# Kernel tuning notes

Hardware: AMD Instinct MI355X
Metric: run time of the kernel (lower is better)

## Reference

```python
import jax, jax.numpy as jnp
import numpy as np

B, S, D = 16, 2048, 256

def setup_inputs() -> dict:
    key = jax.random.key(0)
    ks = jax.random.split(key, 7)
    scale = 1.0 / np.sqrt(D)
    return {
        "x": jax.random.normal(ks[0], (B, S, D), dtype=jnp.float32),
        "Wq": jax.random.normal(ks[1], (D, D), dtype=jnp.float32) * scale,
        "bq": jax.random.normal(ks[2], (D,), dtype=jnp.float32) * 0.01,
        "Wk": jax.random.normal(ks[3], (D, D), dtype=jnp.float32) * scale,
        "bk": jax.random.normal(ks[4], (D,), dtype=jnp.float32) * 0.01,
        "Wv": jax.random.normal(ks[5], (D, D), dtype=jnp.float32) * scale,
        "bv": jax.random.normal(ks[6], (D,), dtype=jnp.float32) * 0.01,
    }

def reference(x, Wq, bq, Wk, bk, Wv, bv):
    # q,k,v: [B,S,D]
    q = x @ Wq + bq
    k = x @ Wk + bk
    v = x @ Wv + bv
    inv_sqrt_d = jnp.asarray(1.0 / np.sqrt(x.shape[-1]), dtype=x.dtype)
    energy = jnp.einsum('bqd,bkd->bqk', q, k) * inv_sqrt_d  # [B,S,S]
    attn = jax.nn.softmax(energy, axis=-1)
    weighted = jnp.einsum('bqk,bkd->bqd', attn, v)  # [B,S,D]
    return weighted.sum(axis=1)  # [B,D]
```

## Files before the change

kernel.cpp:

```cpp
#include <hip/hip_runtime.h>
#include <hip/hip_bf16.h>

typedef __bf16 bf16_t;
typedef bf16_t bf16x8 __attribute__((ext_vector_type(8)));
typedef bf16_t bf16x4 __attribute__((ext_vector_type(4)));
typedef float  f32x4  __attribute__((ext_vector_type(4)));

constexpr int S = 2048, D = 256;


__device__ __forceinline__ float fast_exp2(float x) {
    return __builtin_amdgcn_exp2f(x);
}

__global__ void wt_kernel(const float* __restrict__ Wq, const float* __restrict__ Wk,
                          bf16_t* __restrict__ wtf) {
    int idx = blockIdx.x * 256 + threadIdx.x;
    int w    = idx >> 13;
    int rem  = idx & 8191;
    int nt   = rem >> 9;
    int rem2 = rem & 511;
    int ks   = rem2 >> 6;
    int lane = rem2 & 63;
    int lm = lane & 15, lg = lane >> 4;
    const float* Wsrc = (w == 0) ? Wq : Wk;
    int col = nt * 16 + lm, krow = ks * 32 + lg * 8;
    bf16x8 o;
#pragma unroll
    for (int j = 0; j < 8; j++) o[j] = (bf16_t)Wsrc[(krow + j) * 256 + col];
    *(bf16x8*)(wtf + (size_t)idx * 8) = o;
}

__global__ __launch_bounds__(256) void xconv_kernel(
    const float* __restrict__ x, bf16_t* __restrict__ xf) {
    __shared__ bf16_t xt[4][4096];
    int tid = threadIdx.x, wave = tid >> 6, lane = tid & 63;
    int qb = blockIdx.x * 4 + wave;
    const float* xr = x + (size_t)qb * 16 * 256;
    bf16_t* buf = xt[wave];
    int ks = lane >> 3, lg = (lane & 7) >> 1, j = (lane & 1) * 4;
#pragma unroll
    for (int rr = 0; rr < 16; rr++) {
        float4 f = *(const float4*)(xr + rr * 256 + lane * 4);
        bf16x4 o;
        o[0] = (bf16_t)f.x; o[1] = (bf16_t)f.y; o[2] = (bf16_t)f.z; o[3] = (bf16_t)f.w;
        *(bf16x4*)&buf[(ks * 64 + lg * 16 + rr) * 8 + j] = o;
    }
    bf16_t* dst = xf + (size_t)qb * 4096;
#pragma unroll
    for (int k2 = 0; k2 < 8; k2++) {
        bf16x8 v = *(const bf16x8*)&buf[k2 * 512 + lane * 8];
        *(bf16x8*)(dst + k2 * 512 + lane * 8) = v;
    }
}

__global__ __launch_bounds__(256, 2) void proj_kernel(
    const bf16_t* __restrict__ xf, const bf16_t* __restrict__ wtf,
    const float* __restrict__ bq, const float* __restrict__ bk,
    bf16_t* __restrict__ qo, bf16_t* __restrict__ ko) {
    __shared__ bf16_t bst[32768];
    __shared__ bf16_t sb_all[4][1152];
    int w    = blockIdx.y;
    int tid  = threadIdx.x;
    int wave = tid >> 6, lane = tid & 63, lm = lane & 15, lg = lane >> 4;
    int rowb = blockIdx.x >> 1;
    int colh = blockIdx.x & 1;
    int rowg = wave >> 1, colg = wave & 1;
    const float* bias = (w == 0) ? bq : bk;

    {
        const bf16_t* src = wtf + w * 65536 + (size_t)colh * 32768;
#pragma unroll
        for (int rnd = 0; rnd < 4; rnd++) {
            bf16x8 tmp[4];
#pragma unroll
            for (int u = 0; u < 4; u++)
                tmp[u] = *(const bf16x8*)(src + (size_t)((rnd * 4 + u) * 256 + tid) * 8);
#pragma unroll
            for (int u = 0; u < 4; u++)
                *(bf16x8*)&bst[(size_t)((rnd * 4 + u) * 256 + tid) * 8] = tmp[u];
        }
    }

    int qb0 = rowb * 8 + rowg * 4;
    bf16x8 af[4][8];
#pragma unroll
    for (int s = 0; s < 4; s++) {
        const bf16_t* ab = xf + (size_t)(qb0 + s) * 4096;
#pragma unroll
        for (int ks = 0; ks < 8; ks++)
            af[s][ks] = *(const bf16x8*)(ab + ks * 512 + lane * 8);
    }
    __syncthreads();

    f32x4 acc[4][4];
#pragma unroll
    for (int s = 0; s < 4; s++)
#pragma unroll
        for (int nt = 0; nt < 4; nt++) acc[s][nt] = f32x4{0.f, 0.f, 0.f, 0.f};
#pragma unroll
    for (int ks = 0; ks < 8; ks++) {
#pragma unroll
        for (int nt = 0; nt < 4; nt++) {
            bf16x8 bfr = *(const bf16x8*)&bst[(size_t)(((colg * 4 + nt) * 8 + ks) * 512) + lane * 8];
#pragma unroll
            for (int s = 0; s < 4; s++)
                acc[s][nt] = __builtin_amdgcn_mfma_f32_16x16x32_bf16(af[s][ks], bfr, acc[s][nt], 0, 0, 0);
        }
    }

    bf16_t* sb = sb_all[wave];
    bf16_t* dst = (w == 0) ? qo : ko;
    int c0 = colh * 128 + colg * 64;
#pragma unroll
    for (int s = 0; s < 4; s++) {
#pragma unroll
        for (int nt = 0; nt < 4; nt++) {
            int colloc = nt * 16 + lm;
            float bval = bias[c0 + colloc];
#pragma unroll
            for (int r = 0; r < 4; r++)
                sb[(lg * 4 + r) * 72 + colloc] = (bf16_t)(acc[s][nt][r] + bval);
        }
#pragma unroll
        for (int kk = 0; kk < 2; kk++) {
            bf16x8 v8 = *(const bf16x8*)&sb[lm * 72 + kk * 32 + lg * 8];
            *(bf16x8*)(dst + ((size_t)((qb0 + s) * 8 + (c0 >> 5) + kk)) * 512 + lane * 8) = v8;
        }
    }
}

template <int PASS>
__global__ __launch_bounds__(256) void attn_pass(
    const bf16_t* __restrict__ q, const bf16_t* __restrict__ kmat,
    float* __restrict__ lpart, float* __restrict__ wpart) {
    __shared__ bf16_t kst[2][16384];
    __shared__ float  wacc[4][512];

    int tid  = threadIdx.x;
    int wave = tid >> 6, lane = tid & 63, lm = lane & 15, lg = lane >> 4;
    int i    = blockIdx.x;
    int b    = (i & 7) * 2 + ((i >> 8) & 1);
    int qt   = (i >> 3) & 7;
    int kh   = (i >> 6) & 3;

    bf16x8 af[4][8];
#pragma unroll
    for (int s = 0; s < 4; s++) {
        const bf16_t* qb = q + ((size_t)((b * 128 + qt * 16 + wave * 4 + s) * 8)) * 512;
#pragma unroll
        for (int ks = 0; ks < 8; ks++)
            af[s][ks] = *(const bf16x8*)(qb + ks * 512 + lane * 8);
    }

    constexpr float SCL = 0.0625f * 1.44269504f;

    float lr[4][4];
    if (PASS == 2) {
#pragma unroll
        for (int s = 0; s < 4; s++)
#pragma unroll
            for (int r = 0; r < 4; r++) {
                int row = qt * 256 + wave * 64 + s * 16 + lg * 4 + r;
                float l = 0.f;
#pragma unroll
                for (int k2 = 0; k2 < 4; k2++)
                    l += lpart[(size_t)(k2 * 16 + b) * 2048 + row];
                lr[s][r] = -__builtin_log2f(l);
            }
    }

    float lsum[4][4];
#pragma unroll
    for (int s = 0; s < 4; s++)
#pragma unroll
        for (int r = 0; r < 4; r++) lsum[s][r] = 0.f;

    const bf16_t* kb_base = kmat + (size_t)(b * 128 + kh * 32) * 4096;

    bf16x8 stg[8];
#pragma unroll
    for (int u = 0; u < 8; u++)
        stg[u] = *(const bf16x8*)(kb_base + (size_t)(u * 256 + tid) * 8);

    for (int t = 0; t < 8; t++) {
        int p = t & 1;
#pragma unroll
        for (int u = 0; u < 8; u++)
            *(bf16x8*)&kst[p][(u * 256 + tid) * 8] = stg[u];
        if (t < 7) {
#pragma unroll
            for (int u = 0; u < 8; u++)
                stg[u] = *(const bf16x8*)(kb_base + (size_t)(t + 1) * 16384 + (u * 256 + tid) * 8);
        }
        __syncthreads();

#pragma unroll
        for (int h = 0; h < 2; h++) {
            f32x4 sacc[4][2];
#pragma unroll
            for (int s = 0; s < 4; s++) {
                sacc[s][0] = f32x4{0.f, 0.f, 0.f, 0.f};
                sacc[s][1] = f32x4{0.f, 0.f, 0.f, 0.f};
            }
#pragma unroll
            for (int ks = 0; ks < 8; ks++) {
                bf16x8 b0 = *(const bf16x8*)&kst[p][((h * 2 + 0) * 8 + ks) * 512 + lane * 8];
                bf16x8 b1 = *(const bf16x8*)&kst[p][((h * 2 + 1) * 8 + ks) * 512 + lane * 8];
#pragma unroll
                for (int s = 0; s < 4; s++) {
                    sacc[s][0] = __builtin_amdgcn_mfma_f32_16x16x32_bf16(af[s][ks], b0, sacc[s][0], 0, 0, 0);
                    sacc[s][1] = __builtin_amdgcn_mfma_f32_16x16x32_bf16(af[s][ks], b1, sacc[s][1], 0, 0, 0);
                }
            }
            if (PASS == 1) {
#pragma unroll
                for (int s = 0; s < 4; s++)
#pragma unroll
                    for (int j = 0; j < 2; j++)
#pragma unroll
                        for (int r = 0; r < 4; r++)
                            lsum[s][r] += fast_exp2(sacc[s][j][r] * SCL);
            } else {
#pragma unroll
                for (int j = 0; j < 2; j++) {
                    float wv = 0.f;
#pragma unroll
                    for (int s = 0; s < 4; s++)
#pragma unroll
                        for (int r = 0; r < 4; r++)
                            wv += fast_exp2(__builtin_fmaf(sacc[s][j][r], SCL, lr[s][r]));
                    wv += __shfl_xor(wv, 16);
                    wv += __shfl_xor(wv, 32);
                    if (lg == 0) wacc[wave][t * 64 + (h * 2 + j) * 16 + lm] = wv;
                }
            }
        }
        __syncthreads();
    }

    if (PASS == 1) {
#pragma unroll
        for (int s = 0; s < 4; s++)
#pragma unroll
            for (int r = 0; r < 4; r++) {
                float v2 = lsum[s][r];
                v2 += __shfl_xor(v2, 1);
                v2 += __shfl_xor(v2, 2);
                v2 += __shfl_xor(v2, 4);
                v2 += __shfl_xor(v2, 8);
                if (lm == 0) {
                    int row = qt * 256 + wave * 64 + s * 16 + lg * 4 + r;
                    lpart[(size_t)(kh * 16 + b) * 2048 + row] = v2;
                }
            }
    } else {
#pragma unroll
        for (int u = 0; u < 2; u++) {
            int key = u * 256 + tid;
            float sum = wacc[0][key] + wacc[1][key] + wacc[2][key] + wacc[3][key];
            wpart[(size_t)(qt * 16 + b) * 2048 + kh * 512 + key] = sum;
        }
    }
}

__global__ __launch_bounds__(256) void xsum_kernel(
    const float* __restrict__ wpart, const float* __restrict__ x,
    float* __restrict__ gpart) {
    __shared__ float ldsw[128];
    int b = blockIdx.x >> 4, kseg = blockIdx.x & 15, tid = threadIdx.x;
    if (tid < 128) {
        int key = kseg * 128 + tid;
        float s = 0.f;
#pragma unroll
        for (int qt = 0; qt < 8; qt++) s += wpart[(size_t)(qt * 16 + b) * 2048 + key];
        ldsw[tid] = s;
    }
    __syncthreads();
    const float* xb = x + ((size_t)b * 2048 + kseg * 128) * 256;
    float acc = 0.f;
#pragma unroll 8
    for (int t = 0; t < 128; t++) acc += ldsw[t] * xb[(size_t)t * 256 + tid];
    gpart[(size_t)(kseg * 16 + b) * 256 + tid] = acc;
}

__global__ __launch_bounds__(256) void final_kernel(
    const float* __restrict__ gpart, const float* __restrict__ Wv,
    const float* __restrict__ bv, float* __restrict__ out) {
    __shared__ float yl[256];
    int b = blockIdx.x, tid = threadIdx.x;
    float s = 0.f;
#pragma unroll
    for (int ks = 0; ks < 16; ks++) s += gpart[(size_t)(ks * 16 + b) * 256 + tid];
    yl[tid] = s;
    __syncthreads();
    float acc = 0.f;
#pragma unroll 4
    for (int c = 0; c < 256; c++) acc += yl[c] * Wv[c * 256 + tid];
    out[b * 256 + tid] = acc + 2048.0f * bv[tid];
}

extern "C" void kernel_launch(void* const* d_in, const int* in_sizes, int n_in,
                              void* d_out, int out_size, void* d_ws, size_t ws_size,
                              hipStream_t stream) {
    const float* x  = (const float*)d_in[0];
    const float* Wq = (const float*)d_in[1];
    const float* bq = (const float*)d_in[2];
    const float* Wk = (const float*)d_in[3];
    const float* bk = (const float*)d_in[4];
    const float* Wv = (const float*)d_in[5];
    const float* bv = (const float*)d_in[6];
    float* out = (float*)d_out;

    char* ws = (char*)d_ws;
    bf16_t* wtf   = (bf16_t*)(ws);
    bf16_t* xf    = (bf16_t*)(ws + 262144);
    bf16_t* q     = (bf16_t*)(ws + 17039360);
    bf16_t* kmat  = (bf16_t*)(ws + 33816576);
    float*  lpart = (float*) (ws + 50593792);
    float*  wpart = (float*) (ws + 51118080);
    float*  gpart = (float*) (ws + 52166656);

    wt_kernel<<<dim3(64), dim3(256), 0, stream>>>(Wq, Wk, wtf);
    xconv_kernel<<<dim3(512), dim3(256), 0, stream>>>(x, xf);
    proj_kernel<<<dim3(512, 2), dim3(256), 0, stream>>>(xf, wtf, bq, bk, q, kmat);
    attn_pass<1><<<dim3(512), dim3(256), 0, stream>>>(q, kmat, lpart, wpart);
    attn_pass<2><<<dim3(512), dim3(256), 0, stream>>>(q, kmat, lpart, wpart);
    xsum_kernel<<<dim3(256), dim3(256), 0, stream>>>(wpart, x, gpart);
    final_kernel<<<dim3(16), dim3(256), 0, stream>>>(gpart, Wv, bv, out);
}
```

Before: 204.1 us.

## Split attention key range into 16 chunks per block, load K tile once

The attention passes now split the key dimension into 16 chunks of 128 keys instead of 4 chunks of 512, launching 2048 blocks instead of 512. Each block loads its whole 128-key K tile into shared memory once, replacing the double-buffered streaming loop and its per-tile barriers. The aim is better occupancy and more parallelism across the GPU's CUs. In exchange, each block reloads the Q fragments for fewer keys, and pass 2 reads 16 partial row sums per row instead of 4. The lpart buffer grows, so the workspace offsets move.

```diff
diff --git a/kernel.cpp b/kernel.cpp
--- a/kernel.cpp
+++ b/kernel.cpp
@@ -134,15 +134,26 @@
 __global__ __launch_bounds__(256) void attn_pass(
     const bf16_t* __restrict__ q, const bf16_t* __restrict__ kmat,
     float* __restrict__ lpart, float* __restrict__ wpart) {
-    __shared__ bf16_t kst[2][16384];
-    __shared__ float  wacc[4][512];
+    __shared__ bf16_t kst[32768];
+    __shared__ float  wacc[4][128];
 
     int tid  = threadIdx.x;
     int wave = tid >> 6, lane = tid & 63, lm = lane & 15, lg = lane >> 4;
     int i    = blockIdx.x;
-    int b    = (i & 7) * 2 + ((i >> 8) & 1);
+    int b    = (i & 7) * 2 + ((i >> 10) & 1);
     int qt   = (i >> 3) & 7;
-    int kh   = (i >> 6) & 3;
+    int kh   = (i >> 6) & 15;
+
+    {
+        const bf16_t* src = kmat + (size_t)(b * 128 + kh * 8) * 4096;
+        bf16x8 stg[16];
+#pragma unroll
+        for (int u = 0; u < 16; u++)
+            stg[u] = *(const bf16x8*)(src + (size_t)(u * 256 + tid) * 8);
+#pragma unroll
+        for (int u = 0; u < 16; u++)
+            *(bf16x8*)&kst[(u * 256 + tid) * 8] = stg[u];
+    }
 
     bf16x8 af[4][8];
 #pragma unroll
@@ -164,7 +175,7 @@
                 int row = qt * 256 + wave * 64 + s * 16 + lg * 4 + r;
                 float l = 0.f;
 #pragma unroll
-                for (int k2 = 0; k2 < 4; k2++)
+                for (int k2 = 0; k2 < 16; k2++)
                     l += lpart[(size_t)(k2 * 16 + b) * 2048 + row];
                 lr[s][r] = -__builtin_log2f(l);
             }
@@ -176,67 +187,48 @@
 #pragma unroll
         for (int r = 0; r < 4; r++) lsum[s][r] = 0.f;
 
-    const bf16_t* kb_base = kmat + (size_t)(b * 128 + kh * 32) * 4096;
-
-    bf16x8 stg[8];
-#pragma unroll
-    for (int u = 0; u < 8; u++)
-        stg[u] = *(const bf16x8*)(kb_base + (size_t)(u * 256 + tid) * 8);
-
-    for (int t = 0; t < 8; t++) {
-        int p = t & 1;
-#pragma unroll
-        for (int u = 0; u < 8; u++)
-            *(bf16x8*)&kst[p][(u * 256 + tid) * 8] = stg[u];
-        if (t < 7) {
-#pragma unroll
-            for (int u = 0; u < 8; u++)
-                stg[u] = *(const bf16x8*)(kb_base + (size_t)(t + 1) * 16384 + (u * 256 + tid) * 8);
-        }
-        __syncthreads();
-
-#pragma unroll
-        for (int h = 0; h < 2; h++) {
-            f32x4 sacc[4][2];
+    __syncthreads();
+
+#pragma unroll
+    for (int kp = 0; kp < 4; kp++) {
+        f32x4 sacc[4][2];
+#pragma unroll
+        for (int s = 0; s < 4; s++) {
+            sacc[s][0] = f32x4{0.f, 0.f, 0.f, 0.f};
+            sacc[s][1] = f32x4{0.f, 0.f, 0.f, 0.f};
+        }
+#pragma unroll
+        for (int ks = 0; ks < 8; ks++) {
+            bf16x8 b0 = *(const bf16x8*)&kst[((kp * 2 + 0) * 8 + ks) * 512 + lane * 8];
+            bf16x8 b1 = *(const bf16x8*)&kst[((kp * 2 + 1) * 8 + ks) * 512 + lane * 8];
 #pragma unroll
             for (int s = 0; s < 4; s++) {
-                sacc[s][0] = f32x4{0.f, 0.f, 0.f, 0.f};
-                sacc[s][1] = f32x4{0.f, 0.f, 0.f, 0.f};
+                sacc[s][0] = __builtin_amdgcn_mfma_f32_16x16x32_bf16(af[s][ks], b0, sacc[s][0], 0, 0, 0);
+                sacc[s][1] = __builtin_amdgcn_mfma_f32_16x16x32_bf16(af[s][ks], b1, sacc[s][1], 0, 0, 0);
             }
-#pragma unroll
-            for (int ks = 0; ks < 8; ks++) {
-                bf16x8 b0 = *(const bf16x8*)&kst[p][((h * 2 + 0) * 8 + ks) * 512 + lane * 8];
-                bf16x8 b1 = *(const bf16x8*)&kst[p][((h * 2 + 1) * 8 + ks) * 512 + lane * 8];
-#pragma unroll
-                for (int s = 0; s < 4; s++) {
-                    sacc[s][0] = __builtin_amdgcn_mfma_f32_16x16x32_bf16(af[s][ks], b0, sacc[s][0], 0, 0, 0);
-                    sacc[s][1] = __builtin_amdgcn_mfma_f32_16x16x32_bf16(af[s][ks], b1, sacc[s][1], 0, 0, 0);
-                }
+        }
+        if (PASS == 1) {
+#pragma unroll
+            for (int s = 0; s < 4; s++)
+#pragma unroll
+                for (int j = 0; j < 2; j++)
+#pragma unroll
+                    for (int r = 0; r < 4; r++)
+                        lsum[s][r] += fast_exp2(sacc[s][j][r] * SCL);
+        } else {
+#pragma unroll
+            for (int j = 0; j < 2; j++) {
+                float wv = 0.f;
+#pragma unroll
+                for (int s = 0; s < 4; s++)
+#pragma unroll
+                    for (int r = 0; r < 4; r++)
+                        wv += fast_exp2(__builtin_fmaf(sacc[s][j][r], SCL, lr[s][r]));
+                wv += __shfl_xor(wv, 16);
+                wv += __shfl_xor(wv, 32);
+                if (lg == 0) wacc[wave][kp * 32 + j * 16 + lm] = wv;
             }
-            if (PASS == 1) {
-#pragma unroll
-                for (int s = 0; s < 4; s++)
-#pragma unroll
-                    for (int j = 0; j < 2; j++)
-#pragma unroll
-                        for (int r = 0; r < 4; r++)
-                            lsum[s][r] += fast_exp2(sacc[s][j][r] * SCL);
-            } else {
-#pragma unroll
-                for (int j = 0; j < 2; j++) {
-                    float wv = 0.f;
-#pragma unroll
-                    for (int s = 0; s < 4; s++)
-#pragma unroll
-                        for (int r = 0; r < 4; r++)
-                            wv += fast_exp2(__builtin_fmaf(sacc[s][j][r], SCL, lr[s][r]));
-                    wv += __shfl_xor(wv, 16);
-                    wv += __shfl_xor(wv, 32);
-                    if (lg == 0) wacc[wave][t * 64 + (h * 2 + j) * 16 + lm] = wv;
-                }
-            }
-        }
-        __syncthreads();
+        }
     }
 
     if (PASS == 1) {
@@ -255,11 +247,10 @@
                 }
             }
     } else {
-#pragma unroll
-        for (int u = 0; u < 2; u++) {
-            int key = u * 256 + tid;
-            float sum = wacc[0][key] + wacc[1][key] + wacc[2][key] + wacc[3][key];
-            wpart[(size_t)(qt * 16 + b) * 2048 + kh * 512 + key] = sum;
+        __syncthreads();
+        if (tid < 128) {
+            float sum = wacc[0][tid] + wacc[1][tid] + wacc[2][tid] + wacc[3][tid];
+            wpart[(size_t)(qt * 16 + b) * 2048 + kh * 128 + tid] = sum;
         }
     }
 }
@@ -318,14 +309,14 @@
     bf16_t* q     = (bf16_t*)(ws + 17039360);
     bf16_t* kmat  = (bf16_t*)(ws + 33816576);
     float*  lpart = (float*) (ws + 50593792);
-    float*  wpart = (float*) (ws + 51118080);
-    float*  gpart = (float*) (ws + 52166656);
+    float*  wpart = (float*) (ws + 52690944);
+    float*  gpart = (float*) (ws + 53739520);
 
     wt_kernel<<<dim3(64), dim3(256), 0, stream>>>(Wq, Wk, wtf);
     xconv_kernel<<<dim3(512), dim3(256), 0, stream>>>(x, xf);
     proj_kernel<<<dim3(512, 2), dim3(256), 0, stream>>>(xf, wtf, bq, bk, q, kmat);
-    attn_pass<1><<<dim3(512), dim3(256), 0, stream>>>(q, kmat, lpart, wpart);
-    attn_pass<2><<<dim3(512), dim3(256), 0, stream>>>(q, kmat, lpart, wpart);
+    attn_pass<1><<<dim3(2048), dim3(256), 0, stream>>>(q, kmat, lpart, wpart);
+    attn_pass<2><<<dim3(2048), dim3(256), 0, stream>>>(q, kmat, lpart, wpart);
     xsum_kernel<<<dim3(256), dim3(256), 0, stream>>>(wpart, x, gpart);
     final_kernel<<<dim3(16), dim3(256), 0, stream>>>(gpart, Wv, bv, out);
 }
```

New measurement: 257.4 us. +26.1%, slower.
